# Kernel tuning notes

Measured on AMD Instinct MI355X. Metric: run time of the kernel, lower is better.

The kernel has to match this reference:

```python
import jax, jax.numpy as jnp
import numpy as np

B, C, Wd, Ht = 16, 256, 64, 64
C2 = C // 2

def setup_inputs() -> dict:
    key = jax.random.key(0)
    ks = jax.random.split(key, 9)
    s = 0.05  # keep logits in a sane range (d_qk=128)
    return {
        "x": jax.random.normal(ks[0], (B, C, Wd, Ht), jnp.float32),
        "y": jax.random.normal(ks[1], (B, C, Wd, Ht), jnp.float32),
        "Wq": jax.random.normal(ks[2], (C2, C), jnp.float32) * s,
        "bq": jax.random.normal(ks[3], (C2,), jnp.float32) * s,
        "Wk": jax.random.normal(ks[4], (C2, C), jnp.float32) * s,
        "bk": jax.random.normal(ks[5], (C2,), jnp.float32) * s,
        "Wv": jax.random.normal(ks[6], (C, C), jnp.float32) * s,
        "bv": jax.random.normal(ks[7], (C,), jnp.float32) * s,
        "gamma": jax.random.normal(ks[8], (1,), jnp.float32),
    }

def reference(x, y, Wq, bq, Wk, bk, Wv, bv, gamma):
    b, c, w, h = x.shape
    n = w * h
    xf = x.reshape(b, c, n)           # (B, C, N)
    yf = y.reshape(b, c, n)           # (B, C, N)
    # conv1x1 == channel matmul
    q = jnp.einsum('oc,bcn->bno', Wq, xf) + bq                    # (B, N, C2)
    k = jnp.einsum('oc,bcn->bon', Wk, yf) + bk[None, :, None]     # (B, C2, N)
    energy = jnp.einsum('bno,bom->bnm', q, k)                     # (B, N, N)
    attn = jax.nn.softmax(energy, axis=-1)
    v = jnp.einsum('oc,bcn->bon', Wv, yf) + bv[None, :, None]     # (B, C, N)
    out = jnp.einsum('bon,bmn->bom', v, attn)                     # V @ attn^T
    out = out.reshape(b, c, w, h)
    return gamma[0] * out + y
```

## Files before the change

kernel.cpp:

```cpp
#include <hip/hip_runtime.h>
#include <stdint.h>

using f32x4  = __attribute__((ext_vector_type(4))) float;
using f32x16 = __attribute__((ext_vector_type(16))) float;
using f16x8  = __attribute__((ext_vector_type(8))) _Float16;

#define NB  16
#define NC  256
#define NC2 128
#define NN  4096
#define TILE_B 49152
#define LOG2E 1.44269504f

__device__ __forceinline__ unsigned int pk2(float a, float b) {
    auto h = __builtin_amdgcn_cvt_pkrtz(a, b);
    return __builtin_bit_cast(unsigned int, h);
}

__device__ __forceinline__ f16x8 pack8(f32x4 a, f32x4 b) {
    union { unsigned int w[4]; f16x8 v; } u;
    u.w[0] = pk2(a[0], a[1]); u.w[1] = pk2(a[2], a[3]);
    u.w[2] = pk2(b[0], b[1]); u.w[3] = pk2(b[2], b[3]);
    return u.v;
}

__device__ __forceinline__ void gload16(const void* g, void* l) {
    __builtin_amdgcn_global_load_lds(
        (const __attribute__((address_space(1))) unsigned int*)g,
        (__attribute__((address_space(3))) unsigned int*)l, 16, 0, 0);
}

__global__ __launch_bounds__(256, 2) void qkv_kernel(
    const float* __restrict__ x, const float* __restrict__ y,
    const float* __restrict__ Wq, const float* __restrict__ bq,
    const float* __restrict__ Wk, const float* __restrict__ bk,
    const float* __restrict__ Wv, const float* __restrict__ bv,
    unsigned short* __restrict__ Qf, char* __restrict__ KV)
{
    __shared__ __align__(16) char lds[65536];

    const int bid   = blockIdx.x;
    const int ntile = bid & 63;
    const int bb    = bid >> 6;
    const int nblk  = ntile * 64;

    const int t    = threadIdx.x;
    const int lane = t & 63;
    const int wid  = t >> 6;
    const int l31  = lane & 31;
    const int s    = lane >> 5;

    {
        const bool isQ = (wid < 2);
        const float* srcb = (isQ ? x : y) + (size_t)bb * NC * NN;
        const float* W    = isQ ? Wq : Wk;
        const float* bias = isQ ? bq : bk;
        const int wo = (wid & 1) * 64;
        const int base = isQ ? 49152 : 0;
        const float osc = isQ ? LOG2E : 1.0f;

        f32x16 acc[2][2];
        #pragma unroll
        for (int a = 0; a < 2; ++a)
            #pragma unroll
            for (int bc = 0; bc < 2; ++bc) acc[a][bc] = (f32x16)(0.0f);

        #pragma unroll 4
        for (int ks = 0; ks < 16; ++ks) {
            const int c0 = ks * 16 + s * 8;
            f16x8 wf[2], xf[2];
            #pragma unroll
            for (int a = 0; a < 2; ++a) {
                const float* wr = W + (size_t)(wo + a * 32 + l31) * NC + c0;
                wf[a] = pack8(*(const f32x4*)wr, *(const f32x4*)(wr + 4));
            }
            #pragma unroll
            for (int bc = 0; bc < 2; ++bc) {
                const float* xc = srcb + (size_t)c0 * NN + nblk + bc * 32 + l31;
                f32x4 v0, v1;
                v0[0] = xc[0*NN]; v0[1] = xc[1*NN]; v0[2] = xc[2*NN]; v0[3] = xc[3*NN];
                v1[0] = xc[4*NN]; v1[1] = xc[5*NN]; v1[2] = xc[6*NN]; v1[3] = xc[7*NN];
                xf[bc] = pack8(v0, v1);
            }
            #pragma unroll
            for (int a = 0; a < 2; ++a)
                #pragma unroll
                for (int bc = 0; bc < 2; ++bc)
                    acc[a][bc] = __builtin_amdgcn_mfma_f32_32x32x16_f16(
                        wf[a], xf[bc], acc[a][bc], 0, 0, 0);
        }

        #pragma unroll
        for (int a = 0; a < 2; ++a) {
            #pragma unroll
            for (int bc = 0; bc < 2; ++bc) {
                const int nr = bc * 32 + l31;
                #pragma unroll
                for (int g = 0; g < 4; ++g) {
                    const int o0 = wo + a * 32 + 8 * g + 4 * s;
                    const f32x4 bv4 = *(const f32x4*)(bias + o0);
                    union { unsigned int w[2]; uint2 u2; } pk;
                    pk.w[0] = pk2((acc[a][bc][g*4+0] + bv4[0]) * osc,
                                  (acc[a][bc][g*4+1] + bv4[1]) * osc);
                    pk.w[1] = pk2((acc[a][bc][g*4+2] + bv4[2]) * osc,
                                  (acc[a][bc][g*4+3] + bv4[3]) * osc);
                    const int dst = base + nr*256 +
                        (((o0 >> 3) << 4) ^ ((nr & 15) << 4)) + (o0 & 7) * 2;
                    *(uint2*)(lds + dst) = pk.u2;
                }
            }
        }
    }

    {
        const float* srcb = y + (size_t)bb * NC * NN;
        const int wo = wid * 64;

        f32x16 acc[2][2];
        #pragma unroll
        for (int a = 0; a < 2; ++a)
            #pragma unroll
            for (int bc = 0; bc < 2; ++bc) acc[a][bc] = (f32x16)(0.0f);

        #pragma unroll 4
        for (int ks = 0; ks < 16; ++ks) {
            const int c0 = ks * 16 + s * 8;
            f16x8 wf[2], xf[2];
            #pragma unroll
            for (int a = 0; a < 2; ++a) {
                const float* wr = Wv + (size_t)(wo + a * 32 + l31) * NC + c0;
                wf[a] = pack8(*(const f32x4*)wr, *(const f32x4*)(wr + 4));
            }
            #pragma unroll
            for (int bc = 0; bc < 2; ++bc) {
                const float* xc = srcb + (size_t)c0 * NN + nblk + bc * 32 + l31;
                f32x4 v0, v1;
                v0[0] = xc[0*NN]; v0[1] = xc[1*NN]; v0[2] = xc[2*NN]; v0[3] = xc[3*NN];
                v1[0] = xc[4*NN]; v1[1] = xc[5*NN]; v1[2] = xc[6*NN]; v1[3] = xc[7*NN];
                xf[bc] = pack8(v0, v1);
            }
            #pragma unroll
            for (int a = 0; a < 2; ++a)
                #pragma unroll
                for (int bc = 0; bc < 2; ++bc)
                    acc[a][bc] = __builtin_amdgcn_mfma_f32_32x32x16_f16(
                        xf[bc], wf[a], acc[a][bc], 0, 0, 0);
        }

        #pragma unroll
        for (int a = 0; a < 2; ++a) {
            const int o = wo + a * 32 + l31;
            const float bvo = bv[o];
            #pragma unroll
            for (int bc = 0; bc < 2; ++bc) {
                #pragma unroll
                for (int g = 0; g < 4; ++g) {
                    const int nr = bc * 32 + 8 * g + 4 * s;
                    union { unsigned int w[2]; uint2 u2; } pk;
                    pk.w[0] = pk2(acc[a][bc][g*4+0] + bvo, acc[a][bc][g*4+1] + bvo);
                    pk.w[1] = pk2(acc[a][bc][g*4+2] + bvo, acc[a][bc][g*4+3] + bvo);
                    const int dst = 16384 + ((nr >> 3) << 12) + o*16 + (nr & 7) * 2;
                    *(uint2*)(lds + dst) = pk.u2;
                }
            }
        }
    }

    __syncthreads();

    char* kvt = KV + (size_t)(bb*64 + ntile) * TILE_B;
    #pragma unroll
    for (int i = 0; i < 12; ++i) {
        const int off = (i*256 + t) * 16;
        *(uint4*)(kvt + off) = *(const uint4*)(lds + off);
    }
    char* qg = (char*)Qf + ((size_t)(bb*NN + nblk)) * NC2 * 2;
    #pragma unroll
    for (int i = 0; i < 4; ++i) {
        const int g = (i*256 + t) * 16;
        const int sidx = 49152 + (g ^ (((g >> 8) & 15) << 4));
        *(uint4*)(qg + g) = *(const uint4*)(lds + sidx);
    }
}

__global__ __launch_bounds__(256, 2) void attn_kernel(
    const unsigned short* __restrict__ Qf, const char* __restrict__ KV,
    const float* __restrict__ yg, const float* __restrict__ gamma,
    float* __restrict__ outp)
{
    __shared__ __align__(16) char kls[2][16384];
    __shared__ __align__(16) char vls[32768];

    const int bid = ((blockIdx.x & 7) << 6) + (blockIdx.x >> 3);
    const int bb = bid >> 5;
    const int m0 = (bid & 31) * 128;
    const int t    = threadIdx.x;
    const int lane = t & 63;
    const int wv   = t >> 6;
    const int qcol = lane & 31;
    const int s    = lane >> 5;

    f16x8 qf[8];
    {
        const char* qrow = (const char*)Qf +
            (((size_t)bb*NN + m0 + wv*32 + qcol) * NC2) * 2;
        #pragma unroll
        for (int ks = 0; ks < 8; ++ks)
            qf[ks] = *(const f16x8*)(qrow + ks*32 + s*16);
    }

    f32x16 acc[8];
    #pragma unroll
    for (int ob = 0; ob < 8; ++ob) acc[ob] = (f32x16)(0.0f);
    float m_run = -3.0e38f, l_run = 0.0f;

    const char* kvb = KV + (size_t)bb * 64 * TILE_B;

    #pragma unroll
    for (int i = 0; i < 4; ++i)
        gload16(kvb + ((i*256 + t) << 4), kls[0] + ((i*256 + wv*64) << 4));
    #pragma unroll
    for (int i = 0; i < 8; ++i)
        gload16(kvb + 16384 + ((i*256 + t) << 4), vls + ((i*256 + wv*64) << 4));

    #pragma unroll 1
    for (int it = 0; it < 64; ++it) {
        asm volatile("s_waitcnt vmcnt(8)" ::: "memory");
        __builtin_amdgcn_s_barrier();
        asm volatile("" ::: "memory");

        const char* kbuf = kls[it & 1];
        const char* nsrc = kvb + (size_t)((it + 1) & 63) * TILE_B;

        f32x16 sA = (f32x16)(0.0f), sB = (f32x16)(0.0f);
        {
            const int keyA = qcol, keyB = 32 + qcol;
            const int rbA = keyA * 256, rbB = keyB * 256;
            const int swA = (keyA & 15) << 4, swB = (keyB & 15) << 4;
            __builtin_amdgcn_s_setprio(1);
            #pragma unroll
            for (int ks = 0; ks < 8; ++ks) {
                f16x8 kfA = *(const f16x8*)(kbuf + rbA + ((ks*32 + s*16) ^ swA));
                f16x8 kfB = *(const f16x8*)(kbuf + rbB + ((ks*32 + s*16) ^ swB));
                sA = __builtin_amdgcn_mfma_f32_32x32x16_f16(kfA, qf[ks], sA, 0, 0, 0);
                sB = __builtin_amdgcn_mfma_f32_32x32x16_f16(kfB, qf[ks], sB, 0, 0, 0);
            }
            __builtin_amdgcn_s_setprio(0);
        }

        {
            char* kdst = (char*)kls[(it + 1) & 1];
            #pragma unroll
            for (int i = 0; i < 4; ++i)
                gload16(nsrc + ((i*256 + t) << 4), kdst + ((i*256 + wv*64) << 4));
        }

        asm volatile("s_waitcnt vmcnt(4)" ::: "memory");
        __builtin_amdgcn_s_barrier();
        asm volatile("" ::: "memory");

        float pa[16], pb[16];
        {
            float mx[16];
            #pragma unroll
            for (int r = 0; r < 16; ++r) mx[r] = fmaxf(sA[r], sB[r]);
            #pragma unroll
            for (int st = 8; st >= 1; st >>= 1)
                #pragma unroll
                for (int r = 0; r < st; ++r) mx[r] = fmaxf(mx[r], mx[r + st]);
            float pmax = fmaxf(mx[0], __shfl_xor(mx[0], 32));
            if (__any(pmax > m_run + 11.5415603f)) {
                const float mn = fmaxf(m_run, pmax);
                const float sc = __builtin_amdgcn_exp2f(m_run - mn);
                m_run = mn; l_run *= sc;
                #pragma unroll
                for (int ob = 0; ob < 8; ++ob)
                    #pragma unroll
                    for (int r = 0; r < 16; ++r) acc[ob][r] *= sc;
            }
            #pragma unroll
            for (int r = 0; r < 16; ++r) pa[r] = __builtin_amdgcn_exp2f(sA[r] - m_run);
            #pragma unroll
            for (int r = 0; r < 16; ++r) pb[r] = __builtin_amdgcn_exp2f(sB[r] - m_run);
            float sm[16];
            #pragma unroll
            for (int r = 0; r < 16; ++r) sm[r] = pa[r] + pb[r];
            #pragma unroll
            for (int st = 8; st >= 1; st >>= 1)
                #pragma unroll
                for (int r = 0; r < st; ++r) sm[r] += sm[r + st];
            l_run += sm[0] + __shfl_xor(sm[0], 32);
        }

        #pragma unroll
        for (int st4 = 0; st4 < 4; ++st4) {
            const int kb  = st4 >> 1;
            const int ks2 = st4 & 1;
            const float* pp = kb ? pb : pa;
            const int b0 = ks2 * 8;
            unsigned int pA0 = pk2(pp[b0+0], pp[b0+1]);
            unsigned int pA1 = pk2(pp[b0+2], pp[b0+3]);
            unsigned int pB0 = pk2(pp[b0+4], pp[b0+5]);
            unsigned int pB1 = pk2(pp[b0+6], pp[b0+7]);
            const unsigned int lv0 = s ? pB0 : pA0;
            const unsigned int lv1 = s ? pB1 : pA1;
            const unsigned int sd0 = s ? pA0 : pB0;
            const unsigned int sd1 = s ? pA1 : pB1;
            const unsigned int rv0 = (unsigned int)__shfl_xor((int)sd0, 32);
            const unsigned int rv1 = (unsigned int)__shfl_xor((int)sd1, 32);
            union { unsigned int w[4]; f16x8 v; } u;
            u.w[0] = s ? rv0 : lv0;
            u.w[1] = s ? rv1 : lv1;
            u.w[2] = s ? lv0 : rv0;
            u.w[3] = s ? lv1 : rv1;
            const f16x8 pbx = u.v;
            const char* vplane = vls + (((kb<<2) + (ks2<<1) + s) << 12) + qcol*16;
            __builtin_amdgcn_s_setprio(1);
            #pragma unroll
            for (int ob = 0; ob < 8; ++ob) {
                f16x8 vf = *(const f16x8*)(vplane + ob*512);
                acc[ob] = __builtin_amdgcn_mfma_f32_32x32x16_f16(vf, pbx, acc[ob], 0, 0, 0);
            }
            __builtin_amdgcn_s_setprio(0);
        }

        asm volatile("" ::: "memory");
        __builtin_amdgcn_s_barrier();
        asm volatile("" ::: "memory");

        #pragma unroll
        for (int i = 0; i < 8; ++i)
            gload16(nsrc + 16384 + ((i*256 + t) << 4), vls + ((i*256 + wv*64) << 4));
    }
    asm volatile("s_waitcnt vmcnt(0)" ::: "memory");

    const float ga   = gamma[0];
    const float invl = 1.0f / l_run;
    const int n = m0 + wv*32 + qcol;
    #pragma unroll
    for (int ob = 0; ob < 8; ++ob) {
        #pragma unroll
        for (int r = 0; r < 16; ++r) {
            const int o = ob*32 + (r&3) + 8*(r>>2) + 4*s;
            const size_t a = ((size_t)(bb*NC + o))*NN + n;
            outp[a] = fmaf(acc[ob][r]*invl, ga, yg[a]);
        }
    }
}

extern "C" void kernel_launch(void* const* d_in, const int* in_sizes, int n_in,
                              void* d_out, int out_size, void* d_ws, size_t ws_size,
                              hipStream_t stream) {
    (void)in_sizes; (void)n_in; (void)out_size; (void)ws_size;
    const float* x     = (const float*)d_in[0];
    const float* y     = (const float*)d_in[1];
    const float* Wq    = (const float*)d_in[2];
    const float* bq    = (const float*)d_in[3];
    const float* Wk    = (const float*)d_in[4];
    const float* bk    = (const float*)d_in[5];
    const float* Wv    = (const float*)d_in[6];
    const float* bv    = (const float*)d_in[7];
    const float* gamma = (const float*)d_in[8];
    float* out = (float*)d_out;

    unsigned short* Qf = (unsigned short*)d_ws;
    char* KV = (char*)(Qf + (size_t)NB*NN*NC2);

    qkv_kernel<<<dim3(1024), dim3(256), 0, stream>>>(
        x, y, Wq, bq, Wk, bk, Wv, bv, Qf, KV);
    attn_kernel<<<dim3(512), dim3(256), 0, stream>>>(
        Qf, KV, y, gamma, out);
}
```

Measured before the change: 304.5 us.

## Split QKV projection into two block families and compute row sums via MFMA

The projection kernel now launches twice as many blocks: one family computes Q and K, the other computes V. Each block needs only half the LDS, so occupancy can rise to 4 blocks per CU. In the attention kernel, the per-iteration scalar reduction of softmax probabilities plus a cross-lane shuffle is replaced by an extra MFMA against a vector of ones, moving the row-sum work onto the matrix unit. The cost is one additional MFMA per sub-step and an extra 16-register accumulator, and each V-projection block now re-reads y on its own.

```diff
diff --git a/kernel.cpp b/kernel.cpp
--- a/kernel.cpp
+++ b/kernel.cpp
@@ -30,18 +30,19 @@
         (__attribute__((address_space(3))) unsigned int*)l, 16, 0, 0);
 }
 
-__global__ __launch_bounds__(256, 2) void qkv_kernel(
+__global__ __launch_bounds__(256, 4) void qkv_kernel(
     const float* __restrict__ x, const float* __restrict__ y,
     const float* __restrict__ Wq, const float* __restrict__ bq,
     const float* __restrict__ Wk, const float* __restrict__ bk,
     const float* __restrict__ Wv, const float* __restrict__ bv,
     unsigned short* __restrict__ Qf, char* __restrict__ KV)
 {
-    __shared__ __align__(16) char lds[65536];
+    __shared__ __align__(16) char lds[32768];
 
     const int bid   = blockIdx.x;
+    const int fam   = bid >> 10;
     const int ntile = bid & 63;
-    const int bb    = bid >> 6;
+    const int bb    = (bid >> 6) & 15;
     const int nblk  = ntile * 64;
 
     const int t    = threadIdx.x;
@@ -50,13 +51,15 @@
     const int l31  = lane & 31;
     const int s    = lane >> 5;
 
-    {
+    char* kvt = KV + (size_t)(bb*64 + ntile) * TILE_B;
+
+    if (fam == 0) {
         const bool isQ = (wid < 2);
         const float* srcb = (isQ ? x : y) + (size_t)bb * NC * NN;
         const float* W    = isQ ? Wq : Wk;
         const float* bias = isQ ? bq : bk;
         const int wo = (wid & 1) * 64;
-        const int base = isQ ? 49152 : 0;
+        const int base = isQ ? 16384 : 0;
         const float osc = isQ ? LOG2E : 1.0f;
 
         f32x16 acc[2][2];
@@ -110,9 +113,22 @@
                 }
             }
         }
-    }
-
-    {
+
+        __syncthreads();
+
+        #pragma unroll
+        for (int i = 0; i < 4; ++i) {
+            const int off = (i*256 + t) * 16;
+            *(uint4*)(kvt + off) = *(const uint4*)(lds + off);
+        }
+        char* qg = (char*)Qf + ((size_t)(bb*NN + nblk)) * NC2 * 2;
+        #pragma unroll
+        for (int i = 0; i < 4; ++i) {
+            const int g = (i*256 + t) * 16;
+            const int sidx = 16384 + (g ^ (((g >> 8) & 15) << 4));
+            *(uint4*)(qg + g) = *(const uint4*)(lds + sidx);
+        }
+    } else {
         const float* srcb = y + (size_t)bb * NC * NN;
         const int wo = wid * 64;
 
@@ -159,27 +175,19 @@
                     union { unsigned int w[2]; uint2 u2; } pk;
                     pk.w[0] = pk2(acc[a][bc][g*4+0] + bvo, acc[a][bc][g*4+1] + bvo);
                     pk.w[1] = pk2(acc[a][bc][g*4+2] + bvo, acc[a][bc][g*4+3] + bvo);
-                    const int dst = 16384 + ((nr >> 3) << 12) + o*16 + (nr & 7) * 2;
+                    const int dst = ((nr >> 3) << 12) + o*16 + (nr & 7) * 2;
                     *(uint2*)(lds + dst) = pk.u2;
                 }
             }
         }
-    }
-
-    __syncthreads();
-
-    char* kvt = KV + (size_t)(bb*64 + ntile) * TILE_B;
-    #pragma unroll
-    for (int i = 0; i < 12; ++i) {
-        const int off = (i*256 + t) * 16;
-        *(uint4*)(kvt + off) = *(const uint4*)(lds + off);
-    }
-    char* qg = (char*)Qf + ((size_t)(bb*NN + nblk)) * NC2 * 2;
-    #pragma unroll
-    for (int i = 0; i < 4; ++i) {
-        const int g = (i*256 + t) * 16;
-        const int sidx = 49152 + (g ^ (((g >> 8) & 15) << 4));
-        *(uint4*)(qg + g) = *(const uint4*)(lds + sidx);
+
+        __syncthreads();
+
+        #pragma unroll
+        for (int i = 0; i < 8; ++i) {
+            const int off = (i*256 + t) * 16;
+            *(uint4*)(kvt + 16384 + off) = *(const uint4*)(lds + off);
+        }
     }
 }
 
@@ -209,10 +217,19 @@
             qf[ks] = *(const f16x8*)(qrow + ks*32 + s*16);
     }
 
+    f16x8 onesf;
+    {
+        union { unsigned int w[4]; f16x8 v; } uo;
+        uo.w[0] = 0x3C003C00u; uo.w[1] = 0x3C003C00u;
+        uo.w[2] = 0x3C003C00u; uo.w[3] = 0x3C003C00u;
+        onesf = uo.v;
+    }
+
     f32x16 acc[8];
     #pragma unroll
     for (int ob = 0; ob < 8; ++ob) acc[ob] = (f32x16)(0.0f);
-    float m_run = -3.0e38f, l_run = 0.0f;
+    f32x16 acc_l = (f32x16)(0.0f);
+    float m_run = -3.0e38f;
 
     const char* kvb = KV + (size_t)bb * 64 * TILE_B;
 
@@ -272,7 +289,8 @@
             if (__any(pmax > m_run + 11.5415603f)) {
                 const float mn = fmaxf(m_run, pmax);
                 const float sc = __builtin_amdgcn_exp2f(m_run - mn);
-                m_run = mn; l_run *= sc;
+                m_run = mn;
+                acc_l[0] *= sc;
                 #pragma unroll
                 for (int ob = 0; ob < 8; ++ob)
                     #pragma unroll
@@ -282,14 +300,6 @@
             for (int r = 0; r < 16; ++r) pa[r] = __builtin_amdgcn_exp2f(sA[r] - m_run);
             #pragma unroll
             for (int r = 0; r < 16; ++r) pb[r] = __builtin_amdgcn_exp2f(sB[r] - m_run);
-            float sm[16];
-            #pragma unroll
-            for (int r = 0; r < 16; ++r) sm[r] = pa[r] + pb[r];
-            #pragma unroll
-            for (int st = 8; st >= 1; st >>= 1)
-                #pragma unroll
-                for (int r = 0; r < st; ++r) sm[r] += sm[r + st];
-            l_run += sm[0] + __shfl_xor(sm[0], 32);
         }
 
         #pragma unroll
@@ -321,6 +331,7 @@
                 f16x8 vf = *(const f16x8*)(vplane + ob*512);
                 acc[ob] = __builtin_amdgcn_mfma_f32_32x32x16_f16(vf, pbx, acc[ob], 0, 0, 0);
             }
+            acc_l = __builtin_amdgcn_mfma_f32_32x32x16_f16(onesf, pbx, acc_l, 0, 0, 0);
             __builtin_amdgcn_s_setprio(0);
         }
 
@@ -335,7 +346,7 @@
     asm volatile("s_waitcnt vmcnt(0)" ::: "memory");
 
     const float ga   = gamma[0];
-    const float invl = 1.0f / l_run;
+    const float invl = 1.0f / acc_l[0];
     const int n = m0 + wv*32 + qcol;
     #pragma unroll
     for (int ob = 0; ob < 8; ++ob) {
@@ -366,7 +377,7 @@
     unsigned short* Qf = (unsigned short*)d_ws;
     char* KV = (char*)(Qf + (size_t)NB*NN*NC2);
 
-    qkv_kernel<<<dim3(1024), dim3(256), 0, stream>>>(
+    qkv_kernel<<<dim3(2048), dim3(256), 0, stream>>>(
         x, y, Wq, bq, Wk, bk, Wv, bv, Qf, KV);
     attn_kernel<<<dim3(512), dim3(256), 0, stream>>>(
         Qf, KV, y, gamma, out);
```

Measured after the change: 327.5 us. 7.6% more time.

## Read K fragments directly from global and double-buffer V in LDS

Applied to the files above, without the earlier changes.

The projection kernel now writes K in an MFMA-fragment plane layout, so the attention kernel can load K operands straight from global memory instead of staging them through a swizzled LDS buffer. The LDS space freed by dropping the K buffers becomes a second V buffer, and the next V tile is prefetched after a single __syncthreads per iteration. This removes one barrier and the K LDS round-trip per tile. In exchange, global-load latency lands directly on the QK^T MFMAs, and the in-order vmcnt counter may make the K loads wait behind the outstanding V prefetch.

```diff
diff --git a/kernel.cpp b/kernel.cpp
--- a/kernel.cpp
+++ b/kernel.cpp
@@ -56,7 +56,6 @@
         const float* W    = isQ ? Wq : Wk;
         const float* bias = isQ ? bq : bk;
         const int wo = (wid & 1) * 64;
-        const int base = isQ ? 49152 : 0;
         const float osc = isQ ? LOG2E : 1.0f;
 
         f32x16 acc[2][2];
@@ -104,8 +103,13 @@
                                   (acc[a][bc][g*4+1] + bv4[1]) * osc);
                     pk.w[1] = pk2((acc[a][bc][g*4+2] + bv4[2]) * osc,
                                   (acc[a][bc][g*4+3] + bv4[3]) * osc);
-                    const int dst = base + nr*256 +
-                        (((o0 >> 3) << 4) ^ ((nr & 15) << 4)) + (o0 & 7) * 2;
+                    int dst;
+                    if (isQ) {
+                        dst = 49152 + nr*256 +
+                            (((o0 >> 3) << 4) ^ ((nr & 15) << 4)) + (o0 & 7) * 2;
+                    } else {
+                        dst = ((o0 >> 3) << 10) + nr*16 + (o0 & 7) * 2;
+                    }
                     *(uint2*)(lds + dst) = pk.u2;
                 }
             }
@@ -188,8 +192,7 @@
     const float* __restrict__ yg, const float* __restrict__ gamma,
     float* __restrict__ outp)
 {
-    __shared__ __align__(16) char kls[2][16384];
-    __shared__ __align__(16) char vls[32768];
+    __shared__ __align__(16) char vls[2][32768];
 
     const int bid = ((blockIdx.x & 7) << 6) + (blockIdx.x >> 3);
     const int bb = bid >> 5;
@@ -217,47 +220,26 @@
     const char* kvb = KV + (size_t)bb * 64 * TILE_B;
 
     #pragma unroll
-    for (int i = 0; i < 4; ++i)
-        gload16(kvb + ((i*256 + t) << 4), kls[0] + ((i*256 + wv*64) << 4));
-    #pragma unroll
     for (int i = 0; i < 8; ++i)
-        gload16(kvb + 16384 + ((i*256 + t) << 4), vls + ((i*256 + wv*64) << 4));
+        gload16(kvb + 16384 + ((i*256 + t) << 4), vls[0] + ((i*256 + wv*64) << 4));
 
     #pragma unroll 1
     for (int it = 0; it < 64; ++it) {
-        asm volatile("s_waitcnt vmcnt(8)" ::: "memory");
-        __builtin_amdgcn_s_barrier();
-        asm volatile("" ::: "memory");
-
-        const char* kbuf = kls[it & 1];
-        const char* nsrc = kvb + (size_t)((it + 1) & 63) * TILE_B;
+        const char* kglob = kvb + (size_t)it * TILE_B;
 
         f32x16 sA = (f32x16)(0.0f), sB = (f32x16)(0.0f);
         {
-            const int keyA = qcol, keyB = 32 + qcol;
-            const int rbA = keyA * 256, rbB = keyB * 256;
-            const int swA = (keyA & 15) << 4, swB = (keyB & 15) << 4;
             __builtin_amdgcn_s_setprio(1);
             #pragma unroll
             for (int ks = 0; ks < 8; ++ks) {
-                f16x8 kfA = *(const f16x8*)(kbuf + rbA + ((ks*32 + s*16) ^ swA));
-                f16x8 kfB = *(const f16x8*)(kbuf + rbB + ((ks*32 + s*16) ^ swB));
+                const char* pl = kglob + ((ks*2 + s) << 10) + qcol*16;
+                f16x8 kfA = *(const f16x8*)(pl);
+                f16x8 kfB = *(const f16x8*)(pl + 512);
                 sA = __builtin_amdgcn_mfma_f32_32x32x16_f16(kfA, qf[ks], sA, 0, 0, 0);
                 sB = __builtin_amdgcn_mfma_f32_32x32x16_f16(kfB, qf[ks], sB, 0, 0, 0);
             }
             __builtin_amdgcn_s_setprio(0);
         }
-
-        {
-            char* kdst = (char*)kls[(it + 1) & 1];
-            #pragma unroll
-            for (int i = 0; i < 4; ++i)
-                gload16(nsrc + ((i*256 + t) << 4), kdst + ((i*256 + wv*64) << 4));
-        }
-
-        asm volatile("s_waitcnt vmcnt(4)" ::: "memory");
-        __builtin_amdgcn_s_barrier();
-        asm volatile("" ::: "memory");
 
         float pa[16], pb[16];
         {
@@ -292,6 +274,17 @@
             l_run += sm[0] + __shfl_xor(sm[0], 32);
         }
 
+        __syncthreads();
+
+        if (it < 63) {
+            const char* nsrc = kvb + (size_t)(it + 1) * TILE_B + 16384;
+            char* vdst = (char*)vls[(it + 1) & 1];
+            #pragma unroll
+            for (int i = 0; i < 8; ++i)
+                gload16(nsrc + ((i*256 + t) << 4), vdst + ((i*256 + wv*64) << 4));
+        }
+
+        const char* vbuf = vls[it & 1];
         #pragma unroll
         for (int st4 = 0; st4 < 4; ++st4) {
             const int kb  = st4 >> 1;
@@ -314,7 +307,7 @@
             u.w[2] = s ? lv0 : rv0;
             u.w[3] = s ? lv1 : rv1;
             const f16x8 pbx = u.v;
-            const char* vplane = vls + (((kb<<2) + (ks2<<1) + s) << 12) + qcol*16;
+            const char* vplane = vbuf + (((kb<<2) + (ks2<<1) + s) << 12) + qcol*16;
             __builtin_amdgcn_s_setprio(1);
             #pragma unroll
             for (int ob = 0; ob < 8; ++ob) {
@@ -323,16 +316,7 @@
             }
             __builtin_amdgcn_s_setprio(0);
         }
-
-        asm volatile("" ::: "memory");
-        __builtin_amdgcn_s_barrier();
-        asm volatile("" ::: "memory");
-
-        #pragma unroll
-        for (int i = 0; i < 8; ++i)
-            gload16(nsrc + 16384 + ((i*256 + t) << 4), vls + ((i*256 + wv*64) << 4));
-    }
-    asm volatile("s_waitcnt vmcnt(0)" ::: "memory");
+    }
 
     const float ga   = gamma[0];
     const float invl = 1.0f / l_run;
```

Result: slower. 332.1 us (+9.1%).
